# Optimization experiments

Hardware: AMD Instinct MI355X
Metric: run time of the kernel (lower is better)

The kernel has to match this reference:

```python
import jax, jax.numpy as jnp
import numpy as np
from jax import lax

K = 9  # 3x3 kernel points


def _gather(feat, iy, ix):
    """feat: [B,C,H,W]; iy,ix: [B,K,H,W] int32. Zero padding outside bounds.
    Returns [B,C,K,H,W]."""
    B, C, H, W = feat.shape
    valid = ((iy >= 0) & (iy < H) & (ix >= 0) & (ix < W))
    iyc = jnp.clip(iy, 0, H - 1)
    ixc = jnp.clip(ix, 0, W - 1)
    flat = (iyc * W + ixc).reshape(B, 1, -1)            # [B,1,K*H*W]
    g = jnp.take_along_axis(feat.reshape(B, C, H * W), flat, axis=2)
    g = g.reshape(B, C, K, H, W)
    return g * valid[:, None].astype(feat.dtype)


def _bilinear(feat, ys, xs):
    """feat: [B,C,H,W]; ys,xs: [B,K,H,W] float sampling coords -> [B,C,K,H,W]."""
    y0 = jnp.floor(ys)
    x0 = jnp.floor(xs)
    wy = (ys - y0)[:, None]
    wx = (xs - x0)[:, None]
    y0i = y0.astype(jnp.int32)
    x0i = x0.astype(jnp.int32)
    y1i = y0i + 1
    x1i = x0i + 1
    v00 = _gather(feat, y0i, x0i)
    v01 = _gather(feat, y0i, x1i)
    v10 = _gather(feat, y1i, x0i)
    v11 = _gather(feat, y1i, x1i)
    return (v00 * (1 - wy) * (1 - wx) + v01 * (1 - wy) * wx
            + v10 * wy * (1 - wx) + v11 * wy * wx)


def _deform_layer(x, w_off, b_off, w, b, dilation=1):
    """Modulated deformable 3x3 conv, stride 1, padding=dilation (same size)."""
    B, C, H, W = x.shape
    # offset/mask conv (regular 3x3 conv, same padding)
    om = lax.conv_general_dilated(
        x, w_off, window_strides=(1, 1),
        padding=[(dilation, dilation), (dilation, dilation)],
        rhs_dilation=(dilation, dilation),
        dimension_numbers=('NCHW', 'OIHW', 'NCHW')) + b_off[None, :, None, None]
    off = om[:, :2 * K].reshape(B, K, 2, H, W)   # (dy, dx) per kernel point
    mask = jax.nn.sigmoid(om[:, 2 * K:])         # [B,K,H,W]
    dy = off[:, :, 0]
    dx = off[:, :, 1]
    # base kernel grid offsets (-d, 0, +d)
    ky, kx = jnp.meshgrid(jnp.arange(3), jnp.arange(3), indexing='ij')
    base_y = ((ky.reshape(-1) - 1) * dilation).astype(x.dtype)   # [K]
    base_x = ((kx.reshape(-1) - 1) * dilation).astype(x.dtype)
    gy = jnp.arange(H, dtype=x.dtype)
    gx = jnp.arange(W, dtype=x.dtype)
    ys = gy[None, None, :, None] + base_y[None, :, None, None] + dy  # [B,K,H,W]
    xs = gx[None, None, None, :] + base_x[None, :, None, None] + dx
    sampled = _bilinear(x, ys, xs) * mask[:, None]   # [B,C,K,H,W]
    wk = w.reshape(w.shape[0], w.shape[1], K)        # [O,I,K]
    out = jnp.einsum('bikhw,oik->bohw', sampled, wk) + b[None, :, None, None]
    return out


def setup_inputs() -> dict:
    key = jax.random.key(0)
    ks = jax.random.split(key, 16)
    B, C, H, W = 4, 256, 64, 64
    O = 256
    inp = {'x': jax.random.normal(ks[0], (B, C, H, W), jnp.float32)}
    chans = [(C, C), (C, O), (O, O)]  # layer i==num_layers-2 maps in->out
    for i, (ci, co) in enumerate(chans):
        k = jax.random.split(ks[i + 1], 4)
        # offset conv: 27 = 3*K channels (18 offsets + 9 masks); small init
        inp[f'w_off{i}'] = jax.random.normal(k[0], (3 * K, ci, 3, 3), jnp.float32) * 0.01
        inp[f'b_off{i}'] = jnp.zeros((3 * K,), jnp.float32)
        # deform conv weight: kaiming normal, fan_in = ci*K
        std = np.sqrt(2.0 / (ci * K)).astype(np.float32)
        inp[f'w{i}'] = jax.random.normal(k[1], (co, ci, 3, 3), jnp.float32) * std
        inp[f'b{i}'] = jnp.zeros((co,), jnp.float32)
    return inp


def reference(x, w_off0, b_off0, w0, b0, w_off1, b_off1, w1, b1,
              w_off2, b_off2, w2, b2):
    params = [(w_off0, b_off0, w0, b0),
              (w_off1, b_off1, w1, b1),
              (w_off2, b_off2, w2, b2)]
    for (wo, bo, w, b) in params:
        x = jax.nn.relu(_deform_layer(x, wo, bo, w, b, dilation=1))
    return x
```

## Files before the change

kernel.cpp:

```cpp
#include <hip/hip_runtime.h>
#include <math.h>

#define Bn 4
#define Cn 256
#define Hn 64
#define Wn 64
#define On 256
#define HWn 4096
#define Pn 16384
#define Kc 2304

#define LGKM0 0xc07f

typedef _Float16 half8 __attribute__((ext_vector_type(8)));
typedef float floatx4 __attribute__((ext_vector_type(4)));

__global__ void k_init(const float* __restrict__ x, _Float16* __restrict__ act0,
                       const float* __restrict__ w0, const float* __restrict__ w1,
                       const float* __restrict__ w2, const float* __restrict__ wo0,
                       const float* __restrict__ wo1, const float* __restrict__ wo2,
                       _Float16* __restrict__ wtp, _Float16* __restrict__ wbop) {
  int bx = blockIdx.x;
  int tid = threadIdx.x;
  if (bx < 4096) {
    __shared__ float tile[32][33];
    int cx = bx & 127, cy = (bx >> 7) & 7, b = bx >> 10;
    int c0 = cx * 32, r0 = cy * 32;
    int tx = tid & 31, ty = tid >> 5;
    const float* ib = x + (size_t)b * Cn * HWn;
    _Float16* ob = act0 + (size_t)b * Cn * HWn;
#pragma unroll
    for (int i = 0; i < 32; i += 8)
      tile[ty + i][tx] = ib[(size_t)(r0 + ty + i) * HWn + (c0 + tx)];
    __syncthreads();
#pragma unroll
    for (int i = 0; i < 32; i += 8)
      ob[(size_t)(c0 + ty + i) * Cn + (r0 + tx)] = (_Float16)tile[tx][ty + i];
  } else if (bx < 4864) {
    int b2 = bx - 4096;
    int l = b2 >> 8;
    int n = b2 & 255;
    const float* w = (l == 0) ? w0 : (l == 1) ? w1 : w2;
    _Float16* dst = wtp + (size_t)l * 256 * Kc;
    int g = n >> 4, col = n & 15;
    int cq = tid >> 6;
    int kk = tid & 63;
    int kq = kk >> 5;
    int k32 = kk & 31;
    int quad = k32 >> 3;
    int e = k32 & 7;
    const float* src = w + (size_t)n * 2304 + (size_t)tid * 9;
#pragma unroll
    for (int t = 0; t < 9; ++t) {
      int c = t * 4 + cq;
      size_t d = ((size_t)((c * 16 + g) * 2 + kq)) * 512 + (quad * 16 + col) * 8 + e;
      dst[d] = (_Float16)src[t];
    }
  } else {
    int b3 = bx - 4864;
    int l = b3 >> 5;
    int n = b3 & 31;
    const float* w = (l == 0) ? wo0 : (l == 1) ? wo1 : wo2;
    _Float16* dst = wbop + (size_t)l * 36 * 2048;
    int g = n >> 4, col = n & 15;
    int cw = tid >> 6;
    int r = tid & 63;
    int kq = r >> 5;
    int r2 = r & 31;
    int quad = r2 >> 3;
    int e = r2 & 7;
#pragma unroll
    for (int t = 0; t < 9; ++t) {
      int c = t * 4 + cw;
      size_t d = ((size_t)((c * 2 + g) * 2 + kq)) * 512 + (quad * 16 + col) * 8 + e;
      dst[d] = (n < 27) ? (_Float16)w[((size_t)n * 256 + tid) * 9 + t] : (_Float16)0.f;
    }
  }
}

__global__ __launch_bounds__(512) void k_layer(
    const _Float16* __restrict__ xh,
    const _Float16* __restrict__ wbop, const float* __restrict__ boff,
    const _Float16* __restrict__ wtp, const float* __restrict__ bias,
    _Float16* __restrict__ outh, float* __restrict__ outf) {
  __shared__ __align__(16) _Float16 As[2][64][72];
  __shared__ __align__(16) _Float16 Bs[2][16384];
  __shared__ __align__(16) float sampS[64][9][8];

  int bid = blockIdx.x;
  int lb = ((bid & 7) << 5) + (bid >> 3);
  int p0 = lb * 64;
  int tid = threadIdx.x;
  int lane = tid & 63;
  int wave = tid >> 6;
  int quad = lane >> 4;
  int col = lane & 15;

  int ar = tid >> 3;
  int aci = (tid & 7) * 8;

  int p = p0 + ar;
  int bimg = p >> 12;
  int yx = p & 4095;
  int y = yx >> 6, x = yx & 63;

  half8 zero8;
#pragma unroll
  for (int e = 0; e < 8; ++e) zero8[e] = (_Float16)0.f;

  half8 bst[4];
#pragma unroll
  for (int q = 0; q < 4; ++q)
    bst[q] = *(const half8*)(wtp + (size_t)(q * 512 + tid) * 8);

  _Float16* Bo0 = &Bs[0][0];
  _Float16* Bo1 = &Bs[0][2048];
  float* omS = (float*)&Bs[1][0];

  int mi = wave >> 1;
  int ng = wave & 1;

  floatx4 acc1 = (floatx4){0.f, 0.f, 0.f, 0.f};
  half8 ga, gb = zero8;
  int abase = 0;
  bool avalid = false;
  {
    int sy = y - 1, sx = x - 1;
    avalid = (sy >= 0) & (sy < Hn) & (sx >= 0) & (sx < Wn);
    abase = (((bimg * Hn + (avalid ? sy : 0)) * Wn) + (avalid ? sx : 0)) * Cn;
    ga = zero8;
    if (avalid) ga = *(const half8*)(xh + (size_t)abase + aci);
    if (tid < 256) gb = *(const half8*)(wbop + (size_t)tid * 8);
  }

#pragma unroll
  for (int c = 0; c < 36; ++c) {
    int buf = c & 1;
    *(half8*)&As[buf][ar][aci] = ga;
    if (tid < 256) *(half8*)&(buf ? Bo1 : Bo0)[tid * 8] = gb;

    if (c < 35) {
      int cn = c + 1;
      int tn = cn >> 2;
      int cin = (cn & 3) * 64;
      if ((cn & 3) == 0) {
        int sy = y + tn / 3 - 1;
        int sx = x + tn % 3 - 1;
        avalid = (sy >= 0) & (sy < Hn) & (sx >= 0) & (sx < Wn);
        abase = (((bimg * Hn + (avalid ? sy : 0)) * Wn) + (avalid ? sx : 0)) * Cn;
      }
      ga = zero8;
      if (avalid) ga = *(const half8*)(xh + (size_t)abase + cin + aci);
      if (tid < 256) gb = *(const half8*)(wbop + (size_t)cn * 2048 + tid * 8);
    }

    __builtin_amdgcn_s_waitcnt(LGKM0);
    __builtin_amdgcn_s_barrier();

    const _Float16* BoB = buf ? Bo1 : Bo0;
#pragma unroll
    for (int kq = 0; kq < 2; ++kq) {
      half8 af = *(const half8*)&As[buf][mi * 16 + col][kq * 32 + quad * 8];
      half8 bf = *(const half8*)&BoB[(ng * 2 + kq) * 512 + lane * 8];
      acc1 = __builtin_amdgcn_mfma_f32_16x16x32_f16(af, bf, acc1, 0, 0, 0);
    }
  }

  {
    int n1 = ng * 16 + col;
    if (n1 < 27) {
      float bb = boff[n1];
#pragma unroll
      for (int r = 0; r < 4; ++r)
        omS[(mi * 16 + quad * 4 + r) * 33 + n1] = acc1[r] + bb;
    }
  }
  __syncthreads();

  for (int e = tid; e < 576; e += 512) {
    int lp = e / 9;
    int k = e - lp * 9;
    int pp = p0 + lp;
    int bi = pp >> 12;
    int pyx = pp & 4095;
    int py = pyx >> 6, px = pyx & 63;

    float dy = omS[lp * 33 + 2 * k];
    float dx = omS[lp * 33 + 2 * k + 1];
    float m = 1.f / (1.f + expf(-omS[lp * 33 + 18 + k]));

    float ys = (float)(py + k / 3 - 1) + dy;
    float xs = (float)(px + k % 3 - 1) + dx;
    float y0f = floorf(ys), x0f = floorf(xs);
    float wy = ys - y0f, wx = xs - x0f;
    int y0 = (int)y0f, x0 = (int)x0f;
    int y1 = y0 + 1, x1 = x0 + 1;

    bool vy0 = (y0 >= 0) & (y0 < Hn);
    bool vy1 = (y1 >= 0) & (y1 < Hn);
    bool vx0 = (x0 >= 0) & (x0 < Wn);
    bool vx1 = (x1 >= 0) & (x1 < Wn);
    int y0c = min(max(y0, 0), Hn - 1), y1c = min(max(y1, 0), Hn - 1);
    int x0c = min(max(x0, 0), Wn - 1), x1c = min(max(x1, 0), Wn - 1);

    int base = bi * HWn;
    float* s = &sampS[lp][k][0];
    ((int*)s)[0] = (base + y0c * Wn + x0c) * Cn;
    ((int*)s)[1] = (base + y0c * Wn + x1c) * Cn;
    ((int*)s)[2] = (base + y1c * Wn + x0c) * Cn;
    ((int*)s)[3] = (base + y1c * Wn + x1c) * Cn;
    s[4] = (vy0 && vx0) ? m * (1.f - wy) * (1.f - wx) : 0.f;
    s[5] = (vy0 && vx1) ? m * (1.f - wy) * wx : 0.f;
    s[6] = (vy1 && vx0) ? m * wy * (1.f - wx) : 0.f;
    s[7] = (vy1 && vx1) ? m * wy * wx : 0.f;
  }
  __syncthreads();

  int mw = wave >> 2;
  int nw = wave & 3;

  float bj[4];
#pragma unroll
  for (int j = 0; j < 4; ++j) bj[j] = bias[(nw * 4 + j) * 16 + col];

  floatx4 acc[2][4];
#pragma unroll
  for (int i = 0; i < 2; ++i)
#pragma unroll
    for (int j = 0; j < 4; ++j) acc[i][j] = (floatx4){0.f, 0.f, 0.f, 0.f};

  half8 g00, g01, g10, g11;
  int4 ofsS[2];
  float4 wvS[2];

  ofsS[0] = *(const int4*)&sampS[ar][0][0];
  wvS[0] = *(const float4*)&sampS[ar][0][4];
  g00 = *(const half8*)(xh + (size_t)ofsS[0].x + aci);
  g01 = *(const half8*)(xh + (size_t)ofsS[0].y + aci);
  g10 = *(const half8*)(xh + (size_t)ofsS[0].z + aci);
  g11 = *(const half8*)(xh + (size_t)ofsS[0].w + aci);

#pragma unroll
  for (int c = 0; c < 36; ++c) {
    int buf = c & 1;
    int t = c >> 2;
    {
      float4 wv = wvS[t & 1];
      _Float16 h00 = (_Float16)wv.x, h01 = (_Float16)wv.y;
      _Float16 h10 = (_Float16)wv.z, h11 = (_Float16)wv.w;
      half8 r;
#pragma unroll
      for (int e = 0; e < 8; ++e)
        r[e] = g00[e] * h00 + g01[e] * h01 + g10[e] * h10 + g11[e] * h11;
      *(half8*)&As[buf][ar][aci] = r;
    }
#pragma unroll
    for (int q = 0; q < 4; ++q)
      *(half8*)&Bs[buf][(q * 512 + tid) * 8] = bst[q];

    if (c < 35) {
      int cn = c + 1;
      int tn = cn >> 2;
      int cin = (cn & 3) * 64;
      int4 ofs = ofsS[tn & 1];
      int ci = cin + aci;
      g00 = *(const half8*)(xh + (size_t)ofs.x + ci);
      g01 = *(const half8*)(xh + (size_t)ofs.y + ci);
      g10 = *(const half8*)(xh + (size_t)ofs.z + ci);
      g11 = *(const half8*)(xh + (size_t)ofs.w + ci);
      const _Float16* wsrc = wtp + (size_t)cn * 16384;
#pragma unroll
      for (int q = 0; q < 4; ++q)
        bst[q] = *(const half8*)(wsrc + (size_t)(q * 512 + tid) * 8);
    }
    if ((c & 3) == 0 && t + 1 <= 8) {
      int tnl = t + 1;
      ofsS[tnl & 1] = *(const int4*)&sampS[ar][tnl][0];
      wvS[tnl & 1] = *(const float4*)&sampS[ar][tnl][4];
    }

    __builtin_amdgcn_s_waitcnt(LGKM0);
    __builtin_amdgcn_s_barrier();

    half8 af[2][2];
#pragma unroll
    for (int kq = 0; kq < 2; ++kq)
#pragma unroll
      for (int i = 0; i < 2; ++i)
        af[kq][i] = *(const half8*)&As[buf][mw * 32 + i * 16 + col][kq * 32 + quad * 8];

    half8 bf[2][4];
#pragma unroll
    for (int kq = 0; kq < 2; ++kq)
#pragma unroll
      for (int j = 0; j < 4; ++j)
        bf[kq][j] = *(const half8*)&Bs[buf][((nw * 4 + j) * 2 + kq) * 512 + lane * 8];

#pragma unroll
    for (int kq = 0; kq < 2; ++kq)
#pragma unroll
      for (int i = 0; i < 2; ++i)
#pragma unroll
        for (int j = 0; j < 4; ++j)
          acc[i][j] = __builtin_amdgcn_mfma_f32_16x16x32_f16(
              af[kq][i], bf[kq][j], acc[i][j], 0, 0, 0);
  }

#pragma unroll
  for (int i = 0; i < 2; ++i)
#pragma unroll
    for (int j = 0; j < 4; ++j) {
      int n = (nw * 4 + j) * 16 + col;
      if (outf) {
        int pb = p0 + mw * 32 + i * 16 + quad * 4;
        int bi = pb >> 12;
        int pyx = pb & 4095;
        float4 v;
        v.x = fmaxf(acc[i][j][0] + bj[j], 0.f);
        v.y = fmaxf(acc[i][j][1] + bj[j], 0.f);
        v.z = fmaxf(acc[i][j][2] + bj[j], 0.f);
        v.w = fmaxf(acc[i][j][3] + bj[j], 0.f);
        *(float4*)(outf + ((size_t)(bi * On + n)) * HWn + pyx) = v;
      } else {
#pragma unroll
        for (int r = 0; r < 4; ++r) {
          int pp = p0 + mw * 32 + i * 16 + quad * 4 + r;
          float v = fmaxf(acc[i][j][r] + bj[j], 0.f);
          outh[(size_t)pp * On + n] = (_Float16)v;
        }
      }
    }
}

extern "C" void kernel_launch(void* const* d_in, const int* in_sizes, int n_in,
                              void* d_out, int out_size, void* d_ws, size_t ws_size,
                              hipStream_t stream) {
  (void)in_sizes; (void)n_in; (void)out_size; (void)ws_size;
  const float* x = (const float*)d_in[0];

  _Float16* act0h = (_Float16*)d_ws;
  _Float16* act1h = act0h + (size_t)Pn * Cn;
  _Float16* wbop  = act1h + (size_t)Pn * Cn;
  _Float16* wtp   = wbop + (size_t)3 * 36 * 2048;

  k_init<<<4960, 256, 0, stream>>>(
      x, act0h,
      (const float*)d_in[3], (const float*)d_in[7], (const float*)d_in[11],
      (const float*)d_in[1], (const float*)d_in[5], (const float*)d_in[9],
      wtp, wbop);

  _Float16* cur = act0h;
  _Float16* nxt = act1h;
  for (int l = 0; l < 3; ++l) {
    const float* b_off = (const float*)d_in[2 + l * 4];
    const float* b     = (const float*)d_in[4 + l * 4];
    k_layer<<<Pn / 64, 512, 0, stream>>>(
        cur, wbop + (size_t)l * 36 * 2048, b_off,
        wtp + (size_t)l * 256 * Kc, b, nxt,
        (l == 2) ? (float*)d_out : nullptr);
    _Float16* tswap = cur; cur = nxt; nxt = tswap;
  }
}
```

Before: 232.7 us.

## Load MFMA weight fragments directly from global into registers, drop LDS staging

```diff
diff --git a/kernel.cpp b/kernel.cpp
--- a/kernel.cpp
+++ b/kernel.cpp
@@ -84,7 +84,7 @@
     const _Float16* __restrict__ wtp, const float* __restrict__ bias,
     _Float16* __restrict__ outh, float* __restrict__ outf) {
   __shared__ __align__(16) _Float16 As[2][64][72];
-  __shared__ __align__(16) _Float16 Bs[2][16384];
+  __shared__ __align__(16) float omS[64 * 33];
   __shared__ __align__(16) float sampS[64][9][8];
 
   int bid = blockIdx.x;
@@ -108,20 +108,12 @@
 #pragma unroll
   for (int e = 0; e < 8; ++e) zero8[e] = (_Float16)0.f;
 
-  half8 bst[4];
-#pragma unroll
-  for (int q = 0; q < 4; ++q)
-    bst[q] = *(const half8*)(wtp + (size_t)(q * 512 + tid) * 8);
-
-  _Float16* Bo0 = &Bs[0][0];
-  _Float16* Bo1 = &Bs[0][2048];
-  float* omS = (float*)&Bs[1][0];
-
   int mi = wave >> 1;
   int ng = wave & 1;
 
   floatx4 acc1 = (floatx4){0.f, 0.f, 0.f, 0.f};
-  half8 ga, gb = zero8;
+  half8 ga;
+  half8 bo[2][2];
   int abase = 0;
   bool avalid = false;
   {
@@ -130,14 +122,15 @@
     abase = (((bimg * Hn + (avalid ? sy : 0)) * Wn) + (avalid ? sx : 0)) * Cn;
     ga = zero8;
     if (avalid) ga = *(const half8*)(xh + (size_t)abase + aci);
-    if (tid < 256) gb = *(const half8*)(wbop + (size_t)tid * 8);
+#pragma unroll
+    for (int kq = 0; kq < 2; ++kq)
+      bo[0][kq] = *(const half8*)(wbop + (size_t)(ng * 2 + kq) * 512 + lane * 8);
   }
 
 #pragma unroll
   for (int c = 0; c < 36; ++c) {
     int buf = c & 1;
     *(half8*)&As[buf][ar][aci] = ga;
-    if (tid < 256) *(half8*)&(buf ? Bo1 : Bo0)[tid * 8] = gb;
 
     if (c < 35) {
       int cn = c + 1;
@@ -151,18 +144,19 @@
       }
       ga = zero8;
       if (avalid) ga = *(const half8*)(xh + (size_t)abase + cin + aci);
-      if (tid < 256) gb = *(const half8*)(wbop + (size_t)cn * 2048 + tid * 8);
+      const _Float16* wob = wbop + (size_t)cn * 2048;
+#pragma unroll
+      for (int kq = 0; kq < 2; ++kq)
+        bo[cn & 1][kq] = *(const half8*)(wob + (size_t)(ng * 2 + kq) * 512 + lane * 8);
     }
 
     __builtin_amdgcn_s_waitcnt(LGKM0);
     __builtin_amdgcn_s_barrier();
 
-    const _Float16* BoB = buf ? Bo1 : Bo0;
 #pragma unroll
     for (int kq = 0; kq < 2; ++kq) {
       half8 af = *(const half8*)&As[buf][mi * 16 + col][kq * 32 + quad * 8];
-      half8 bf = *(const half8*)&BoB[(ng * 2 + kq) * 512 + lane * 8];
-      acc1 = __builtin_amdgcn_mfma_f32_16x16x32_f16(af, bf, acc1, 0, 0, 0);
+      acc1 = __builtin_amdgcn_mfma_f32_16x16x32_f16(af, bo[buf][kq], acc1, 0, 0, 0);
     }
   }
 
@@ -230,6 +224,7 @@
     for (int j = 0; j < 4; ++j) acc[i][j] = (floatx4){0.f, 0.f, 0.f, 0.f};
 
   half8 g00, g01, g10, g11;
+  half8 bw[2][2][4];
   int4 ofsS[2];
   float4 wvS[2];
 
@@ -239,6 +234,12 @@
   g01 = *(const half8*)(xh + (size_t)ofsS[0].y + aci);
   g10 = *(const half8*)(xh + (size_t)ofsS[0].z + aci);
   g11 = *(const half8*)(xh + (size_t)ofsS[0].w + aci);
+#pragma unroll
+  for (int kq = 0; kq < 2; ++kq)
+#pragma unroll
+    for (int j = 0; j < 4; ++j)
+      bw[0][kq][j] =
+          *(const half8*)(wtp + (size_t)((nw * 4 + j) * 2 + kq) * 512 + lane * 8);
 
 #pragma unroll
   for (int c = 0; c < 36; ++c) {
@@ -254,9 +255,6 @@
         r[e] = g00[e] * h00 + g01[e] * h01 + g10[e] * h10 + g11[e] * h11;
       *(half8*)&As[buf][ar][aci] = r;
     }
-#pragma unroll
-    for (int q = 0; q < 4; ++q)
-      *(half8*)&Bs[buf][(q * 512 + tid) * 8] = bst[q];
 
     if (c < 35) {
       int cn = c + 1;
@@ -270,8 +268,11 @@
       g11 = *(const half8*)(xh + (size_t)ofs.w + ci);
       const _Float16* wsrc = wtp + (size_t)cn * 16384;
 #pragma unroll
-      for (int q = 0; q < 4; ++q)
-        bst[q] = *(const half8*)(wsrc + (size_t)(q * 512 + tid) * 8);
+      for (int kq = 0; kq < 2; ++kq)
+#pragma unroll
+        for (int j = 0; j < 4; ++j)
+          bw[cn & 1][kq][j] =
+              *(const half8*)(wsrc + (size_t)((nw * 4 + j) * 2 + kq) * 512 + lane * 8);
     }
     if ((c & 3) == 0 && t + 1 <= 8) {
       int tnl = t + 1;
@@ -289,13 +290,6 @@
       for (int i = 0; i < 2; ++i)
         af[kq][i] = *(const half8*)&As[buf][mw * 32 + i * 16 + col][kq * 32 + quad * 8];
 
-    half8 bf[2][4];
-#pragma unroll
-    for (int kq = 0; kq < 2; ++kq)
-#pragma unroll
-      for (int j = 0; j < 4; ++j)
-        bf[kq][j] = *(const half8*)&Bs[buf][((nw * 4 + j) * 2 + kq) * 512 + lane * 8];
-
 #pragma unroll
     for (int kq = 0; kq < 2; ++kq)
 #pragma unroll
@@ -303,7 +297,7 @@
 #pragma unroll
         for (int j = 0; j < 4; ++j)
           acc[i][j] = __builtin_amdgcn_mfma_f32_16x16x32_f16(
-              af[kq][i], bf[kq][j], acc[i][j], 0, 0, 0);
+              af[kq][i], bw[buf][kq][j], acc[i][j], 0, 0, 0);
   }
 
 #pragma unroll
```

Result: no change. 234.6 us (+0.8%).

## Restructure offset and deform GEMM loops into rolled 9x4 loops with two-deep weight prefetch

Applied to the files above, without the earlier changes.

```diff
diff --git a/kernel.cpp b/kernel.cpp
--- a/kernel.cpp
+++ b/kernel.cpp
@@ -85,6 +85,7 @@
     _Float16* __restrict__ outh, float* __restrict__ outf) {
   __shared__ __align__(16) _Float16 As[2][64][72];
   __shared__ __align__(16) _Float16 Bs[2][16384];
+  __shared__ __align__(16) float omS[64 * 33];
   __shared__ __align__(16) float sampS[64][9][8];
 
   int bid = blockIdx.x;
@@ -108,20 +109,12 @@
 #pragma unroll
   for (int e = 0; e < 8; ++e) zero8[e] = (_Float16)0.f;
 
-  half8 bst[4];
-#pragma unroll
-  for (int q = 0; q < 4; ++q)
-    bst[q] = *(const half8*)(wtp + (size_t)(q * 512 + tid) * 8);
-
-  _Float16* Bo0 = &Bs[0][0];
-  _Float16* Bo1 = &Bs[0][2048];
-  float* omS = (float*)&Bs[1][0];
-
   int mi = wave >> 1;
   int ng = wave & 1;
 
   floatx4 acc1 = (floatx4){0.f, 0.f, 0.f, 0.f};
-  half8 ga, gb = zero8;
+  half8 ga;
+  half8 bos0, bos1;
   int abase = 0;
   bool avalid = false;
   {
@@ -130,39 +123,46 @@
     abase = (((bimg * Hn + (avalid ? sy : 0)) * Wn) + (avalid ? sx : 0)) * Cn;
     ga = zero8;
     if (avalid) ga = *(const half8*)(xh + (size_t)abase + aci);
-    if (tid < 256) gb = *(const half8*)(wbop + (size_t)tid * 8);
-  }
-
-#pragma unroll
-  for (int c = 0; c < 36; ++c) {
-    int buf = c & 1;
-    *(half8*)&As[buf][ar][aci] = ga;
-    if (tid < 256) *(half8*)&(buf ? Bo1 : Bo0)[tid * 8] = gb;
-
-    if (c < 35) {
-      int cn = c + 1;
-      int tn = cn >> 2;
-      int cin = (cn & 3) * 64;
-      if ((cn & 3) == 0) {
+    bos0 = zero8; bos1 = zero8;
+    if (tid < 256) {
+      bos0 = *(const half8*)(wbop + (size_t)tid * 8);
+      bos1 = *(const half8*)(wbop + 2048 + (size_t)tid * 8);
+    }
+  }
+
+#pragma unroll 1
+  for (int t = 0; t < 9; ++t) {
+#pragma unroll
+    for (int cc = 0; cc < 4; ++cc) {
+      *(half8*)&As[cc & 1][ar][aci] = ga;
+      if (tid < 256)
+        *(half8*)&Bs[cc & 1][tid * 8] = (cc & 1) ? bos1 : bos0;
+      if (cc < 3) {
+        ga = zero8;
+        if (avalid) ga = *(const half8*)(xh + (size_t)abase + (cc + 1) * 64 + aci);
+      } else if (t < 8) {
+        int tn = t + 1;
         int sy = y + tn / 3 - 1;
         int sx = x + tn % 3 - 1;
         avalid = (sy >= 0) & (sy < Hn) & (sx >= 0) & (sx < Wn);
         abase = (((bimg * Hn + (avalid ? sy : 0)) * Wn) + (avalid ? sx : 0)) * Cn;
-      }
-      ga = zero8;
-      if (avalid) ga = *(const half8*)(xh + (size_t)abase + cin + aci);
-      if (tid < 256) gb = *(const half8*)(wbop + (size_t)cn * 2048 + tid * 8);
-    }
-
-    __builtin_amdgcn_s_waitcnt(LGKM0);
-    __builtin_amdgcn_s_barrier();
-
-    const _Float16* BoB = buf ? Bo1 : Bo0;
-#pragma unroll
-    for (int kq = 0; kq < 2; ++kq) {
-      half8 af = *(const half8*)&As[buf][mi * 16 + col][kq * 32 + quad * 8];
-      half8 bf = *(const half8*)&BoB[(ng * 2 + kq) * 512 + lane * 8];
-      acc1 = __builtin_amdgcn_mfma_f32_16x16x32_f16(af, bf, acc1, 0, 0, 0);
+        ga = zero8;
+        if (avalid) ga = *(const half8*)(xh + (size_t)abase + aci);
+      }
+      if ((cc < 2 || t < 8) && tid < 256) {
+        half8 v = *(const half8*)(wbop + ((size_t)(4 * t) + cc + 2) * 2048 + tid * 8);
+        if (cc & 1) bos1 = v; else bos0 = v;
+      }
+
+      __builtin_amdgcn_s_waitcnt(LGKM0);
+      __builtin_amdgcn_s_barrier();
+
+#pragma unroll
+      for (int kq = 0; kq < 2; ++kq) {
+        half8 af = *(const half8*)&As[cc & 1][mi * 16 + col][kq * 32 + quad * 8];
+        half8 bf = *(const half8*)&Bs[cc & 1][(ng * 2 + kq) * 512 + lane * 8];
+        acc1 = __builtin_amdgcn_mfma_f32_16x16x32_f16(af, bf, acc1, 0, 0, 0);
+      }
     }
   }
 
@@ -230,80 +230,95 @@
     for (int j = 0; j < 4; ++j) acc[i][j] = (floatx4){0.f, 0.f, 0.f, 0.f};
 
   half8 g00, g01, g10, g11;
-  int4 ofsS[2];
-  float4 wvS[2];
-
-  ofsS[0] = *(const int4*)&sampS[ar][0][0];
-  wvS[0] = *(const float4*)&sampS[ar][0][4];
-  g00 = *(const half8*)(xh + (size_t)ofsS[0].x + aci);
-  g01 = *(const half8*)(xh + (size_t)ofsS[0].y + aci);
-  g10 = *(const half8*)(xh + (size_t)ofsS[0].z + aci);
-  g11 = *(const half8*)(xh + (size_t)ofsS[0].w + aci);
-
-#pragma unroll
-  for (int c = 0; c < 36; ++c) {
-    int buf = c & 1;
-    int t = c >> 2;
-    {
-      float4 wv = wvS[t & 1];
-      _Float16 h00 = (_Float16)wv.x, h01 = (_Float16)wv.y;
-      _Float16 h10 = (_Float16)wv.z, h11 = (_Float16)wv.w;
-      half8 r;
-#pragma unroll
-      for (int e = 0; e < 8; ++e)
-        r[e] = g00[e] * h00 + g01[e] * h01 + g10[e] * h10 + g11[e] * h11;
-      *(half8*)&As[buf][ar][aci] = r;
-    }
-#pragma unroll
-    for (int q = 0; q < 4; ++q)
-      *(half8*)&Bs[buf][(q * 512 + tid) * 8] = bst[q];
-
-    if (c < 35) {
-      int cn = c + 1;
-      int tn = cn >> 2;
-      int cin = (cn & 3) * 64;
-      int4 ofs = ofsS[tn & 1];
-      int ci = cin + aci;
-      g00 = *(const half8*)(xh + (size_t)ofs.x + ci);
-      g01 = *(const half8*)(xh + (size_t)ofs.y + ci);
-      g10 = *(const half8*)(xh + (size_t)ofs.z + ci);
-      g11 = *(const half8*)(xh + (size_t)ofs.w + ci);
-      const _Float16* wsrc = wtp + (size_t)cn * 16384;
+  half8 bst0[4], bst1[4];
+  int4 ofsC, ofsN;
+  float4 wvC, wvN;
+
+  ofsC = *(const int4*)&sampS[ar][0][0];
+  wvC = *(const float4*)&sampS[ar][0][4];
+  ofsN = ofsC; wvN = wvC;
+  g00 = *(const half8*)(xh + (size_t)ofsC.x + aci);
+  g01 = *(const half8*)(xh + (size_t)ofsC.y + aci);
+  g10 = *(const half8*)(xh + (size_t)ofsC.z + aci);
+  g11 = *(const half8*)(xh + (size_t)ofsC.w + aci);
+#pragma unroll
+  for (int q = 0; q < 4; ++q)
+    bst0[q] = *(const half8*)(wtp + (size_t)(q * 512 + tid) * 8);
+#pragma unroll
+  for (int q = 0; q < 4; ++q)
+    bst1[q] = *(const half8*)(wtp + 16384 + (size_t)(q * 512 + tid) * 8);
+
+#pragma unroll 1
+  for (int t = 0; t < 9; ++t) {
+    if (t < 8) {
+      ofsN = *(const int4*)&sampS[ar][t + 1][0];
+      wvN = *(const float4*)&sampS[ar][t + 1][4];
+    }
+#pragma unroll
+    for (int cc = 0; cc < 4; ++cc) {
+      {
+        _Float16 h00 = (_Float16)wvC.x, h01 = (_Float16)wvC.y;
+        _Float16 h10 = (_Float16)wvC.z, h11 = (_Float16)wvC.w;
+        half8 r;
+#pragma unroll
+        for (int e = 0; e < 8; ++e)
+          r[e] = g00[e] * h00 + g01[e] * h01 + g10[e] * h10 + g11[e] * h11;
+        *(half8*)&As[cc & 1][ar][aci] = r;
+      }
 #pragma unroll
       for (int q = 0; q < 4; ++q)
-        bst[q] = *(const half8*)(wsrc + (size_t)(q * 512 + tid) * 8);
-    }
-    if ((c & 3) == 0 && t + 1 <= 8) {
-      int tnl = t + 1;
-      ofsS[tnl & 1] = *(const int4*)&sampS[ar][tnl][0];
-      wvS[tnl & 1] = *(const float4*)&sampS[ar][tnl][4];
-    }
-
-    __builtin_amdgcn_s_waitcnt(LGKM0);
-    __builtin_amdgcn_s_barrier();
-
-    half8 af[2][2];
-#pragma unroll
-    for (int kq = 0; kq < 2; ++kq)
-#pragma unroll
-      for (int i = 0; i < 2; ++i)
-        af[kq][i] = *(const half8*)&As[buf][mw * 32 + i * 16 + col][kq * 32 + quad * 8];
-
-    half8 bf[2][4];
-#pragma unroll
-    for (int kq = 0; kq < 2; ++kq)
-#pragma unroll
-      for (int j = 0; j < 4; ++j)
-        bf[kq][j] = *(const half8*)&Bs[buf][((nw * 4 + j) * 2 + kq) * 512 + lane * 8];
-
-#pragma unroll
-    for (int kq = 0; kq < 2; ++kq)
-#pragma unroll
-      for (int i = 0; i < 2; ++i)
+        *(half8*)&Bs[cc & 1][(q * 512 + tid) * 8] = (cc & 1) ? bst1[q] : bst0[q];
+      if (cc < 3) {
+        int ci = (cc + 1) * 64 + aci;
+        g00 = *(const half8*)(xh + (size_t)ofsC.x + ci);
+        g01 = *(const half8*)(xh + (size_t)ofsC.y + ci);
+        g10 = *(const half8*)(xh + (size_t)ofsC.z + ci);
+        g11 = *(const half8*)(xh + (size_t)ofsC.w + ci);
+      } else if (t < 8) {
+        g00 = *(const half8*)(xh + (size_t)ofsN.x + aci);
+        g01 = *(const half8*)(xh + (size_t)ofsN.y + aci);
+        g10 = *(const half8*)(xh + (size_t)ofsN.z + aci);
+        g11 = *(const half8*)(xh + (size_t)ofsN.w + aci);
+      }
+      if (cc < 2 || t < 8) {
+        const _Float16* wsrc = wtp + ((size_t)(4 * t) + cc + 2) * 16384;
+#pragma unroll
+        for (int q = 0; q < 4; ++q) {
+          half8 v = *(const half8*)(wsrc + (size_t)(q * 512 + tid) * 8);
+          if (cc & 1) bst1[q] = v; else bst0[q] = v;
+        }
+      }
+
+      __builtin_amdgcn_s_waitcnt(LGKM0);
+      __builtin_amdgcn_s_barrier();
+
+      half8 af[2][2];
+#pragma unroll
+      for (int kq = 0; kq < 2; ++kq)
+#pragma unroll
+        for (int i = 0; i < 2; ++i)
+          af[kq][i] =
+              *(const half8*)&As[cc & 1][mw * 32 + i * 16 + col][kq * 32 + quad * 8];
+
+      half8 bf[2][4];
+#pragma unroll
+      for (int kq = 0; kq < 2; ++kq)
 #pragma unroll
         for (int j = 0; j < 4; ++j)
-          acc[i][j] = __builtin_amdgcn_mfma_f32_16x16x32_f16(
-              af[kq][i], bf[kq][j], acc[i][j], 0, 0, 0);
+          bf[kq][j] =
+              *(const half8*)&Bs[cc & 1][((nw * 4 + j) * 2 + kq) * 512 + lane * 8];
+
+#pragma unroll
+      for (int kq = 0; kq < 2; ++kq)
+#pragma unroll
+        for (int i = 0; i < 2; ++i)
+#pragma unroll
+          for (int j = 0; j < 4; ++j)
+            acc[i][j] = __builtin_amdgcn_mfma_f32_16x16x32_f16(
+                af[kq][i], bf[kq][j], acc[i][j], 0, 0, 0);
+    }
+    ofsC = ofsN;
+    wvC = wvN;
   }
 
 #pragma unroll
```

Result: no change. 232.3 us (-0.2%).
